# Kernel tuning notes

Measured on AMD Instinct MI355X. Metric: run time of the kernel, lower is better.

## Reference

```python
import jax, jax.numpy as jnp
import numpy as np

N, E = 50000, 800000
IN_C, HID, HEADS, NUM_CLASSES = 256, 64, 4, 10
LRELU_SLOPE = 0.2
LN_EPS = 1e-5


def setup_inputs() -> dict:
    key = jax.random.key(0)
    ks = jax.random.split(key, 12)
    HC = HEADS * HID
    glorot = lambda k, shp: jax.random.normal(k, shp, jnp.float32) * np.sqrt(2.0 / (shp[0] + shp[-1]))
    return {
        "x": jax.random.normal(ks[0], (N, IN_C), jnp.float32),
        "edge_index": jax.random.randint(ks[1], (2, E), 0, N, jnp.int64),
        "edge_weight": jax.random.uniform(ks[2], (E, 1), jnp.float32),
        "W": glorot(ks[3], (IN_C, HC)),
        "att_src": glorot(ks[4], (1, HEADS, HID)),
        "att_dst": glorot(ks[5], (1, HEADS, HID)),
        "att_edge": glorot(ks[6], (1, HEADS, HID)),
        "W_edge": glorot(ks[7], (1, HC)),
        "bias": jnp.zeros((HC,), jnp.float32),
        "ln_gamma": jnp.ones((HC,), jnp.float32),
        "ln_beta": jnp.zeros((HC,), jnp.float32),
        "fc_W": glorot(ks[8], (HC, NUM_CLASSES)),
        "fc_b": jnp.zeros((NUM_CLASSES,), jnp.float32),
    }


def reference(x, edge_index, edge_weight, W, att_src, att_dst, att_edge,
              W_edge, bias, ln_gamma, ln_beta, fc_W, fc_b):
    n = x.shape[0]
    src, dst = edge_index[0], edge_index[1]

    # GATConv: linear projection -> [N, H, C]
    xh = (x @ W).reshape(n, HEADS, HID)
    a_src = jnp.sum(xh * att_src, axis=-1)  # [N, H]
    a_dst = jnp.sum(xh * att_dst, axis=-1)  # [N, H]

    # edge feature projection (edge_dim=1) -> per-edge attention term
    eh = (edge_weight @ W_edge).reshape(-1, HEADS, HID)  # [E, H, C]
    a_edge = jnp.sum(eh * att_edge, axis=-1)             # [E, H]

    alpha = a_src[src] + a_dst[dst] + a_edge             # [E, H]
    alpha = jax.nn.leaky_relu(alpha, LRELU_SLOPE)

    # segment softmax over incoming edges of each destination node
    amax = jax.ops.segment_max(alpha, dst, num_segments=n)  # [N, H]
    amax = jnp.where(jnp.isfinite(amax), amax, 0.0)
    ex = jnp.exp(alpha - amax[dst])
    esum = jax.ops.segment_sum(ex, dst, num_segments=n)     # [N, H]
    attn = ex / (esum[dst] + 1e-16)                          # [E, H]

    # message = gathered source features weighted by attention; scatter-add
    msg = xh[src] * attn[:, :, None]                          # [E, H, C]
    out = jax.ops.segment_sum(msg, dst, num_segments=n)      # [N, H, C]
    out = out.reshape(n, HEADS * HID) + bias                  # concat heads

    # LayerNorm + ReLU (dropout is identity in eval) + Linear head
    mu = jnp.mean(out, axis=-1, keepdims=True)
    var = jnp.mean(jnp.square(out - mu), axis=-1, keepdims=True)
    out = (out - mu) * jax.lax.rsqrt(var + LN_EPS) * ln_gamma + ln_beta
    out = jax.nn.relu(out)
    return out @ fc_W + fc_b
```

## Files before the change

kernel.cpp:

```cpp
#include <hip/hip_runtime.h>
#include <hip/hip_bf16.h>

static constexpr int HEADS = 4;
static constexpr int HID   = 64;
static constexpr int HC    = 256;
static constexpr int NCLS  = 10;

typedef short bf16x8 __attribute__((ext_vector_type(8)));
typedef float f32x4  __attribute__((ext_vector_type(4)));
typedef _Float16 f16x4 __attribute__((ext_vector_type(4)));

__device__ inline unsigned short f2bf(float f) {
    union { float f; unsigned u; } c; c.f = f;
    unsigned r = (c.u + 0x7fff + ((c.u >> 16) & 1)) >> 16;
    return (unsigned short)r;
}
__device__ inline unsigned short f2h(float f) {
    _Float16 h = (_Float16)f; unsigned short u; __builtin_memcpy(&u, &h, 2); return u;
}
__device__ inline float h2f(unsigned short u) {
    _Float16 h; __builtin_memcpy(&h, &u, 2); return (float)h;
}

__global__ void prep_kernel(const float* __restrict__ We, const float* __restrict__ attE,
                            float* __restrict__ cE, const float* __restrict__ W,
                            unsigned short* __restrict__ Wt, const float* __restrict__ fcW,
                            float* __restrict__ fcWt) {
    int b = blockIdx.x, t = threadIdx.x;
    if (b == 0) {
        float p = We[t] * attE[t];
#pragma unroll
        for (int d = 32; d; d >>= 1) p += __shfl_xor(p, d, 64);
        if ((t & 63) == 0) cE[t >> 6] = p;
    } else if (b <= 256) {
        int k = b - 1;
        Wt[t * 256 + k] = f2bf(W[k * 256 + t]);
    } else {
        int j = b - 257;
        fcWt[j * HC + t] = fcW[t * NCLS + j];
    }
}

__global__ __launch_bounds__(256) void gemm_mfma(const float* __restrict__ X,
                                                 const unsigned short* __restrict__ Bt,
                                                 unsigned short* __restrict__ XHh, int M) {
    __shared__ alignas(16) unsigned short As[128][40];
    __shared__ alignas(16) unsigned short Bs[128][40];
    const int tid = threadIdx.x;
    const int lane = tid & 63, wid = tid >> 6;
    const int wr = wid >> 1, wc = wid & 1;
    const int bm = blockIdx.x * 128, bn = blockIdx.y * 128;
    const int fr = lane & 15, kg = lane >> 4;

    f32x4 acc[4][4] = {};

    for (int k0 = 0; k0 < 256; k0 += 32) {
        __syncthreads();
#pragma unroll
        for (int ss = 0; ss < 4; ++ss) {
            int idx = tid + (ss << 8);
            int row = idx >> 3, seg = idx & 7;
            int grow = bm + row;
            float4 av = make_float4(0.f, 0.f, 0.f, 0.f);
            if (grow < M) av = *(const float4*)&X[(size_t)grow * 256 + k0 + seg * 4];
            ushort4 ab = make_ushort4(f2bf(av.x), f2bf(av.y), f2bf(av.z), f2bf(av.w));
            *(ushort4*)&As[row][seg * 4] = ab;
        }
#pragma unroll
        for (int qq = 0; qq < 2; ++qq) {
            int q = tid + (qq << 8);
            int row = q >> 2, part = q & 3;
            const ushort4* bp = (const ushort4*)&Bt[(size_t)(bn + row) * 256 + k0 + part * 8];
            *(ushort4*)&Bs[row][part * 8]     = bp[0];
            *(ushort4*)&Bs[row][part * 8 + 4] = bp[1];
        }
        __syncthreads();

        bf16x8 af[4], bf[4];
#pragma unroll
        for (int i = 0; i < 4; ++i)
            af[i] = *(const bf16x8*)&As[wr * 64 + i * 16 + fr][kg * 8];
#pragma unroll
        for (int j = 0; j < 4; ++j)
            bf[j] = *(const bf16x8*)&Bs[wc * 64 + j * 16 + fr][kg * 8];
#pragma unroll
        for (int i = 0; i < 4; ++i)
#pragma unroll
            for (int j = 0; j < 4; ++j)
                acc[i][j] = __builtin_amdgcn_mfma_f32_16x16x32_bf16(af[i], bf[j], acc[i][j], 0, 0, 0);
    }

#pragma unroll
    for (int i = 0; i < 4; ++i) {
#pragma unroll
        for (int j = 0; j < 4; ++j) {
            int col = bn + wc * 64 + j * 16 + fr;
#pragma unroll
            for (int r = 0; r < 4; ++r) {
                int row = bm + wr * 64 + i * 16 + kg * 4 + r;
                if (row < M) XHh[(size_t)row * 256 + col] = f2h(acc[i][j][r]);
            }
        }
    }
}

__global__ __launch_bounds__(256) void attn_coef(const unsigned short* __restrict__ xhh,
                                                 const float* __restrict__ attS,
                                                 const float* __restrict__ attD,
                                                 float* __restrict__ a_src,
                                                 float* __restrict__ a_dst,
                                                 int Nn) {
    int wid = threadIdx.x >> 6, lane = threadIdx.x & 63;
    int n = blockIdx.x * 4 + wid;
    if (n >= Nn) return;
    ushort4 xv = *(const ushort4*)&xhh[(size_t)n * HC + lane * 4];
    float x0 = h2f(xv.x), x1 = h2f(xv.y), x2 = h2f(xv.z), x3 = h2f(xv.w);
    float4 sv = *(const float4*)&attS[lane * 4];
    float4 dv = *(const float4*)&attD[lane * 4];
    float ps = x0 * sv.x + x1 * sv.y + x2 * sv.z + x3 * sv.w;
    float pd = x0 * dv.x + x1 * dv.y + x2 * dv.z + x3 * dv.w;
#pragma unroll
    for (int d = 1; d < 16; d <<= 1) {
        ps += __shfl_xor(ps, d, 64);
        pd += __shfl_xor(pd, d, 64);
    }
    if ((lane & 15) == 0) {
        a_src[n * 4 + (lane >> 4)] = ps;
        a_dst[n * 4 + (lane >> 4)] = pd;
    }
}

__global__ void hist_kernel(const int* __restrict__ dst, int* __restrict__ deg, int E) {
    int e = blockIdx.x * 256 + threadIdx.x;
    if (e < E) atomicAdd(&deg[dst[e]], 1);
}

__global__ __launch_bounds__(1024) void scan1(const int* __restrict__ deg,
                                              int* __restrict__ row_start,
                                              int* __restrict__ bsum, int n) {
    __shared__ int wsum[16];
    const int tid = threadIdx.x, lane = tid & 63, wid = tid >> 6;
    int i = blockIdx.x * 1024 + tid;
    int v = (i < n) ? ((deg[i] + 3) & ~3) : 0;
    int incl = v;
#pragma unroll
    for (int d = 1; d < 64; d <<= 1) {
        int t = __shfl_up(incl, d, 64);
        if (lane >= d) incl += t;
    }
    if (lane == 63) wsum[wid] = incl;
    __syncthreads();
    if (tid < 16) {
        int w = wsum[tid];
#pragma unroll
        for (int d = 1; d < 16; d <<= 1) {
            int t = __shfl_up(w, d, 16);
            if (tid >= d) w += t;
        }
        wsum[tid] = w;
    }
    __syncthreads();
    int waveoff = wid ? wsum[wid - 1] : 0;
    if (i < n) row_start[i] = waveoff + incl - v;
    if (tid == 1023) bsum[blockIdx.x] = waveoff + incl;
}

__global__ __launch_bounds__(1024) void scan23(int* __restrict__ row_start,
                                               const int* __restrict__ bsum,
                                               int* __restrict__ cursor, int n, int nb) {
    __shared__ int pref[64];
    const int tid = threadIdx.x;
    if (tid < 64) {
        int v = (tid < nb) ? bsum[tid] : 0;
#pragma unroll
        for (int d = 1; d < 64; d <<= 1) {
            int t = __shfl_up(v, d, 64);
            if (tid >= d) v += t;
        }
        pref[tid] = v;
    }
    __syncthreads();
    int add = blockIdx.x ? pref[blockIdx.x - 1] : 0;
    int i = blockIdx.x * 1024 + tid;
    if (i < n) {
        int v = row_start[i] + add;
        row_start[i] = v;
        cursor[i] = v;
    }
    if (i == n) row_start[n] = pref[nb - 1];
}

__global__ void scatter_p(const int* __restrict__ src, const int* __restrict__ dst,
                          const float* __restrict__ ew, const float* __restrict__ a_src,
                          const float* __restrict__ a_dst, const float* __restrict__ cE,
                          int* __restrict__ cursor, int* __restrict__ srcs,
                          float* __restrict__ pq, int E) {
    int e = blockIdx.x * 256 + threadIdx.x;
    if (e >= E) return;
    int s = src[e], d = dst[e];
    float w = ew[e];
    float4 as_ = *(const float4*)&a_src[s * 4];
    float4 ad_ = *(const float4*)&a_dst[d * 4];
    float4 ce  = *(const float4*)cE;
    int pos = atomicAdd(&cursor[d], 1);
    srcs[pos] = s;
    float al[4] = {as_.x + ad_.x + ce.x * w, as_.y + ad_.y + ce.y * w,
                   as_.z + ad_.z + ce.z * w, as_.w + ad_.w + ce.w * w};
    float* base = pq + ((size_t)(pos >> 2)) * 16 + (pos & 3);
#pragma unroll
    for (int h = 0; h < 4; ++h) {
        float a = al[h] > 0.f ? al[h] : 0.2f * al[h];
        base[h * 4] = __expf(a);
    }
}

__global__ __launch_bounds__(256) void gat_main(
    const unsigned short* __restrict__ xhh, const int* __restrict__ row_start,
    const int* __restrict__ srcs, const float* __restrict__ pq,
    const float* __restrict__ bias, const float* __restrict__ gamma,
    const float* __restrict__ beta, const float* __restrict__ fcWt,
    const float* __restrict__ fcb, float* __restrict__ out, int Nn) {
    const int lane = threadIdx.x & 63, wid = threadIdx.x >> 6;
    const int n = blockIdx.x * 4 + wid;
    if (n >= Nn) return;
    const int myh = lane >> 4;
    const int rs = row_start[n], re = row_start[n + 1];

    f32x4 acc = {0.f, 0.f, 0.f, 0.f};
    float psum = 0.f;

    if (rs < re) {
        int4   sv = *(const int4*)&srcs[rs];
        float4 pv = *(const float4*)&pq[((size_t)(rs >> 2)) * 16 + myh * 4];
        for (int e0 = rs; e0 < re; e0 += 4) {
            int e1 = e0 + 4;
            int4 svn = sv; float4 pvn = pv;
            if (e1 < re) {
                svn = *(const int4*)&srcs[e1];
                pvn = *(const float4*)&pq[((size_t)(e1 >> 2)) * 16 + myh * 4];
            }
            psum += ((pv.x + pv.y) + (pv.z + pv.w));
            {
                int sb = __builtin_amdgcn_readfirstlane(sv.x);
                f16x4 xv = *(const f16x4*)(xhh + (size_t)sb * HC + lane * 4);
                acc[0] = fmaf(pv.x, (float)xv.x, acc[0]);
                acc[1] = fmaf(pv.x, (float)xv.y, acc[1]);
                acc[2] = fmaf(pv.x, (float)xv.z, acc[2]);
                acc[3] = fmaf(pv.x, (float)xv.w, acc[3]);
            }
            {
                int sb = __builtin_amdgcn_readfirstlane(sv.y);
                f16x4 xv = *(const f16x4*)(xhh + (size_t)sb * HC + lane * 4);
                acc[0] = fmaf(pv.y, (float)xv.x, acc[0]);
                acc[1] = fmaf(pv.y, (float)xv.y, acc[1]);
                acc[2] = fmaf(pv.y, (float)xv.z, acc[2]);
                acc[3] = fmaf(pv.y, (float)xv.w, acc[3]);
            }
            {
                int sb = __builtin_amdgcn_readfirstlane(sv.z);
                f16x4 xv = *(const f16x4*)(xhh + (size_t)sb * HC + lane * 4);
                acc[0] = fmaf(pv.z, (float)xv.x, acc[0]);
                acc[1] = fmaf(pv.z, (float)xv.y, acc[1]);
                acc[2] = fmaf(pv.z, (float)xv.z, acc[2]);
                acc[3] = fmaf(pv.z, (float)xv.w, acc[3]);
            }
            {
                int sb = __builtin_amdgcn_readfirstlane(sv.w);
                f16x4 xv = *(const f16x4*)(xhh + (size_t)sb * HC + lane * 4);
                acc[0] = fmaf(pv.w, (float)xv.x, acc[0]);
                acc[1] = fmaf(pv.w, (float)xv.y, acc[1]);
                acc[2] = fmaf(pv.w, (float)xv.z, acc[2]);
                acc[3] = fmaf(pv.w, (float)xv.w, acc[3]);
            }
            sv = svn; pv = pvn;
        }
    }

    float rin = 1.f / (psum + 1e-16f);

    float4 bv = *(const float4*)&bias[lane * 4];
    float v0 = acc[0] * rin + bv.x;
    float v1 = acc[1] * rin + bv.y;
    float v2 = acc[2] * rin + bv.z;
    float v3 = acc[3] * rin + bv.w;

    float s1 = v0 + v1 + v2 + v3;
    float s2 = v0 * v0 + v1 * v1 + v2 * v2 + v3 * v3;
#pragma unroll
    for (int d = 1; d < 64; d <<= 1) {
        s1 += __shfl_xor(s1, d, 64);
        s2 += __shfl_xor(s2, d, 64);
    }
    float mu = s1 * (1.f / 256.f);
    float var = s2 * (1.f / 256.f) - mu * mu;
    float rstd = rsqrtf(var + 1e-5f);
    float4 gv = *(const float4*)&gamma[lane * 4];
    float4 btv = *(const float4*)&beta[lane * 4];
    float y0 = fmaxf((v0 - mu) * rstd * gv.x + btv.x, 0.f);
    float y1 = fmaxf((v1 - mu) * rstd * gv.y + btv.y, 0.f);
    float y2 = fmaxf((v2 - mu) * rstd * gv.z + btv.z, 0.f);
    float y3 = fmaxf((v3 - mu) * rstd * gv.w + btv.w, 0.f);

    float keep = 0.f;
#pragma unroll
    for (int j = 0; j < NCLS; ++j) {
        float4 wv = *(const float4*)&fcWt[j * HC + lane * 4];
        float pj = y0 * wv.x;
        pj = fmaf(y1, wv.y, pj);
        pj = fmaf(y2, wv.z, pj);
        pj = fmaf(y3, wv.w, pj);
#pragma unroll
        for (int d = 1; d < 64; d <<= 1) pj += __shfl_xor(pj, d, 64);
        if (lane == j) keep = pj + fcb[j];
    }
    if (lane < NCLS) out[n * NCLS + lane] = keep;
}

extern "C" void kernel_launch(void* const* d_in, const int* in_sizes, int n_in,
                              void* d_out, int out_size, void* d_ws, size_t ws_size,
                              hipStream_t stream) {
    const float* x    = (const float*)d_in[0];
    const int*   ei   = (const int*)d_in[1];
    const float* ew   = (const float*)d_in[2];
    const float* W    = (const float*)d_in[3];
    const float* attS = (const float*)d_in[4];
    const float* attD = (const float*)d_in[5];
    const float* attE = (const float*)d_in[6];
    const float* We   = (const float*)d_in[7];
    const float* bias = (const float*)d_in[8];
    const float* gam  = (const float*)d_in[9];
    const float* bet  = (const float*)d_in[10];
    const float* fcW  = (const float*)d_in[11];
    const float* fcb  = (const float*)d_in[12];
    float* out = (float*)d_out;

    const int Nn = in_sizes[0] / HC;
    const int E  = in_sizes[1] / 2;
    const int* src = ei;
    const int* dst = ei + E;
    const int nb = (Nn + 1023) / 1024;
    const int EpMax = E + 4 * Nn;

    char* ws = (char*)d_ws;
    size_t off = 0;
    auto alloc = [&](size_t bytes) { void* p = ws + off; off = (off + bytes + 255) & ~size_t(255); return p; };
    unsigned short* xhh  = (unsigned short*)alloc((size_t)Nn * HC * 2);
    unsigned short* wt   = (unsigned short*)alloc((size_t)HC * HC * 2);
    float* a_srcb    = (float*)alloc((size_t)Nn * 4 * 4);
    float* a_dstb    = (float*)alloc((size_t)Nn * 4 * 4);
    float* cE        = (float*)alloc(256);
    float* fcWt      = (float*)alloc((size_t)NCLS * HC * 4);
    int*   row_start = (int*)  alloc((size_t)(Nn + 1) * 4);
    int*   deg       = (int*)  alloc((size_t)Nn * 4);
    int*   cursor    = (int*)  alloc((size_t)Nn * 4);
    int*   bsum      = (int*)  alloc((size_t)nb * 4);
    int*   srcs     = (int*)  alloc((size_t)EpMax * 4);
    float* pq       = (float*)alloc((size_t)EpMax * 16);
    (void)ws_size;

    hipMemsetAsync(deg, 0, (size_t)Nn * 4, stream);
    size_t zspan = (size_t)((char*)pq - (char*)srcs) + (size_t)EpMax * 16;
    hipMemsetAsync(srcs, 0, zspan, stream);

    prep_kernel<<<267, 256, 0, stream>>>(We, attE, cE, W, wt, fcW, fcWt);

    dim3 g((Nn + 127) / 128, 2);
    gemm_mfma<<<g, 256, 0, stream>>>(x, wt, xhh, Nn);

    attn_coef<<<(Nn + 3) / 4, 256, 0, stream>>>(xhh, attS, attD, a_srcb, a_dstb, Nn);
    hist_kernel<<<(E + 255) / 256, 256, 0, stream>>>(dst, deg, E);
    scan1<<<nb, 1024, 0, stream>>>(deg, row_start, bsum, Nn);
    scan23<<<nb, 1024, 0, stream>>>(row_start, bsum, cursor, Nn, nb);
    scatter_p<<<(E + 255) / 256, 256, 0, stream>>>(src, dst, ew, a_srcb, a_dstb, cE,
                                                   cursor, srcs, pq, E);
    gat_main<<<(Nn + 3) / 4, 256, 0, stream>>>(xhh, row_start, srcs, pq,
                                               bias, gam, bet, fcWt, fcb, out, Nn);
}
```

Measured before the change: 220.1 us.

## Precompute edge ranks, pipeline gathers, drop memset, split FC into MFMA kernel

The histogram pass now records each edge's rank within its destination, so the scatter computes slot positions without a second atomic pass, and the cursor array goes away. The large memset of srcs/pq is removed, and the tail of each padded row is handled by masking instead. The gather loop is restructured into a two-stage software pipeline that prefetches the next 4-edge chunk's features and the metadata two chunks ahead. The per-node FC reduction, which used ten wave-wide shuffle reductions, is replaced by writing fp16 LayerNorm output and running a separate MFMA GEMM kernel. This costs an extra 25MB round trip for yh and fp16 rounding of the activations.

```diff
diff --git a/kernel.cpp b/kernel.cpp
--- a/kernel.cpp
+++ b/kernel.cpp
@@ -6,9 +6,10 @@
 static constexpr int HC    = 256;
 static constexpr int NCLS  = 10;
 
-typedef short bf16x8 __attribute__((ext_vector_type(8)));
-typedef float f32x4  __attribute__((ext_vector_type(4)));
-typedef _Float16 f16x4 __attribute__((ext_vector_type(4)));
+typedef short    bf16x8 __attribute__((ext_vector_type(8)));
+typedef _Float16 f16x8  __attribute__((ext_vector_type(8)));
+typedef _Float16 f16x4  __attribute__((ext_vector_type(4)));
+typedef float    f32x4  __attribute__((ext_vector_type(4)));
 
 __device__ inline unsigned short f2bf(float f) {
     union { float f; unsigned u; } c; c.f = f;
@@ -25,7 +26,7 @@
 __global__ void prep_kernel(const float* __restrict__ We, const float* __restrict__ attE,
                             float* __restrict__ cE, const float* __restrict__ W,
                             unsigned short* __restrict__ Wt, const float* __restrict__ fcW,
-                            float* __restrict__ fcWt) {
+                            unsigned short* __restrict__ fcWh) {
     int b = blockIdx.x, t = threadIdx.x;
     if (b == 0) {
         float p = We[t] * attE[t];
@@ -37,7 +38,9 @@
         Wt[t * 256 + k] = f2bf(W[k * 256 + t]);
     } else {
         int j = b - 257;
-        fcWt[j * HC + t] = fcW[t * NCLS + j];
+        unsigned short v = 0;
+        if (j < NCLS) v = f2h(fcW[t * NCLS + j]);
+        fcWh[j * 256 + t] = v;
     }
 }
 
@@ -130,9 +133,10 @@
     }
 }
 
-__global__ void hist_kernel(const int* __restrict__ dst, int* __restrict__ deg, int E) {
+__global__ void hist_kernel(const int* __restrict__ dst, int* __restrict__ deg,
+                            int* __restrict__ rank, int E) {
     int e = blockIdx.x * 256 + threadIdx.x;
-    if (e < E) atomicAdd(&deg[dst[e]], 1);
+    if (e < E) rank[e] = atomicAdd(&deg[dst[e]], 1);
 }
 
 __global__ __launch_bounds__(1024) void scan1(const int* __restrict__ deg,
@@ -166,8 +170,7 @@
 }
 
 __global__ __launch_bounds__(1024) void scan23(int* __restrict__ row_start,
-                                               const int* __restrict__ bsum,
-                                               int* __restrict__ cursor, int n, int nb) {
+                                               const int* __restrict__ bsum, int n, int nb) {
     __shared__ int pref[64];
     const int tid = threadIdx.x;
     if (tid < 64) {
@@ -182,19 +185,15 @@
     __syncthreads();
     int add = blockIdx.x ? pref[blockIdx.x - 1] : 0;
     int i = blockIdx.x * 1024 + tid;
-    if (i < n) {
-        int v = row_start[i] + add;
-        row_start[i] = v;
-        cursor[i] = v;
-    }
+    if (i < n) row_start[i] += add;
     if (i == n) row_start[n] = pref[nb - 1];
 }
 
 __global__ void scatter_p(const int* __restrict__ src, const int* __restrict__ dst,
                           const float* __restrict__ ew, const float* __restrict__ a_src,
                           const float* __restrict__ a_dst, const float* __restrict__ cE,
-                          int* __restrict__ cursor, int* __restrict__ srcs,
-                          float* __restrict__ pq, int E) {
+                          const int* __restrict__ row_start, const int* __restrict__ rank,
+                          int* __restrict__ srcs, float* __restrict__ pq, int E) {
     int e = blockIdx.x * 256 + threadIdx.x;
     if (e >= E) return;
     int s = src[e], d = dst[e];
@@ -202,7 +201,7 @@
     float4 as_ = *(const float4*)&a_src[s * 4];
     float4 ad_ = *(const float4*)&a_dst[d * 4];
     float4 ce  = *(const float4*)cE;
-    int pos = atomicAdd(&cursor[d], 1);
+    int pos = row_start[d] + rank[e];
     srcs[pos] = s;
     float al[4] = {as_.x + ad_.x + ce.x * w, as_.y + ad_.y + ce.y * w,
                    as_.z + ad_.z + ce.z * w, as_.w + ad_.w + ce.w * w};
@@ -216,65 +215,82 @@
 
 __global__ __launch_bounds__(256) void gat_main(
     const unsigned short* __restrict__ xhh, const int* __restrict__ row_start,
-    const int* __restrict__ srcs, const float* __restrict__ pq,
-    const float* __restrict__ bias, const float* __restrict__ gamma,
-    const float* __restrict__ beta, const float* __restrict__ fcWt,
-    const float* __restrict__ fcb, float* __restrict__ out, int Nn) {
+    const int* __restrict__ deg, const int* __restrict__ srcs,
+    const float* __restrict__ pq, const float* __restrict__ bias,
+    const float* __restrict__ gamma, const float* __restrict__ beta,
+    unsigned short* __restrict__ yh, int Nn) {
     const int lane = threadIdx.x & 63, wid = threadIdx.x >> 6;
     const int n = blockIdx.x * 4 + wid;
     if (n >= Nn) return;
     const int myh = lane >> 4;
-    const int rs = row_start[n], re = row_start[n + 1];
+    const int rs = row_start[n];
+    const int dn = deg[n];
+    const int nfull = dn >> 2, rem = dn & 3;
+    const unsigned short* xl = xhh + (size_t)lane * 4;
 
     f32x4 acc = {0.f, 0.f, 0.f, 0.f};
     float psum = 0.f;
 
-    if (rs < re) {
-        int4   sv = *(const int4*)&srcs[rs];
-        float4 pv = *(const float4*)&pq[((size_t)(rs >> 2)) * 16 + myh * 4];
-        for (int e0 = rs; e0 < re; e0 += 4) {
-            int e1 = e0 + 4;
-            int4 svn = sv; float4 pvn = pv;
-            if (e1 < re) {
-                svn = *(const int4*)&srcs[e1];
-                pvn = *(const float4*)&pq[((size_t)(e1 >> 2)) * 16 + myh * 4];
-            }
-            psum += ((pv.x + pv.y) + (pv.z + pv.w));
-            {
-                int sb = __builtin_amdgcn_readfirstlane(sv.x);
-                f16x4 xv = *(const f16x4*)(xhh + (size_t)sb * HC + lane * 4);
-                acc[0] = fmaf(pv.x, (float)xv.x, acc[0]);
-                acc[1] = fmaf(pv.x, (float)xv.y, acc[1]);
-                acc[2] = fmaf(pv.x, (float)xv.z, acc[2]);
-                acc[3] = fmaf(pv.x, (float)xv.w, acc[3]);
-            }
-            {
-                int sb = __builtin_amdgcn_readfirstlane(sv.y);
-                f16x4 xv = *(const f16x4*)(xhh + (size_t)sb * HC + lane * 4);
-                acc[0] = fmaf(pv.y, (float)xv.x, acc[0]);
-                acc[1] = fmaf(pv.y, (float)xv.y, acc[1]);
-                acc[2] = fmaf(pv.y, (float)xv.z, acc[2]);
-                acc[3] = fmaf(pv.y, (float)xv.w, acc[3]);
-            }
-            {
-                int sb = __builtin_amdgcn_readfirstlane(sv.z);
-                f16x4 xv = *(const f16x4*)(xhh + (size_t)sb * HC + lane * 4);
-                acc[0] = fmaf(pv.z, (float)xv.x, acc[0]);
-                acc[1] = fmaf(pv.z, (float)xv.y, acc[1]);
-                acc[2] = fmaf(pv.z, (float)xv.z, acc[2]);
-                acc[3] = fmaf(pv.z, (float)xv.w, acc[3]);
-            }
-            {
-                int sb = __builtin_amdgcn_readfirstlane(sv.w);
-                f16x4 xv = *(const f16x4*)(xhh + (size_t)sb * HC + lane * 4);
-                acc[0] = fmaf(pv.w, (float)xv.x, acc[0]);
-                acc[1] = fmaf(pv.w, (float)xv.y, acc[1]);
-                acc[2] = fmaf(pv.w, (float)xv.z, acc[2]);
-                acc[3] = fmaf(pv.w, (float)xv.w, acc[3]);
-            }
-            sv = svn; pv = pvn;
-        }
-    }
+#define LOADMETA(c, S, P)                                                     \
+    S = *(const int4*)&srcs[rs + (c) * 4];                                    \
+    P = *(const float4*)&pq[((size_t)((rs >> 2) + (c))) * 16 + myh * 4];
+#define GATHER(S, X0, X1, X2, X3)                                             \
+    X0 = *(const f16x4*)(xl + (size_t)__builtin_amdgcn_readfirstlane((S).x) * HC); \
+    X1 = *(const f16x4*)(xl + (size_t)__builtin_amdgcn_readfirstlane((S).y) * HC); \
+    X2 = *(const f16x4*)(xl + (size_t)__builtin_amdgcn_readfirstlane((S).z) * HC); \
+    X3 = *(const f16x4*)(xl + (size_t)__builtin_amdgcn_readfirstlane((S).w) * HC);
+#define COMPUTE(P, X0, X1, X2, X3)                                            \
+    psum += ((P).x + (P).y) + ((P).z + (P).w);                                \
+    acc[0] = fmaf((P).x, (float)(X0).x, acc[0]);                              \
+    acc[1] = fmaf((P).x, (float)(X0).y, acc[1]);                              \
+    acc[2] = fmaf((P).x, (float)(X0).z, acc[2]);                              \
+    acc[3] = fmaf((P).x, (float)(X0).w, acc[3]);                              \
+    acc[0] = fmaf((P).y, (float)(X1).x, acc[0]);                              \
+    acc[1] = fmaf((P).y, (float)(X1).y, acc[1]);                              \
+    acc[2] = fmaf((P).y, (float)(X1).z, acc[2]);                              \
+    acc[3] = fmaf((P).y, (float)(X1).w, acc[3]);                              \
+    acc[0] = fmaf((P).z, (float)(X2).x, acc[0]);                              \
+    acc[1] = fmaf((P).z, (float)(X2).y, acc[1]);                              \
+    acc[2] = fmaf((P).z, (float)(X2).z, acc[2]);                              \
+    acc[3] = fmaf((P).z, (float)(X2).w, acc[3]);                              \
+    acc[0] = fmaf((P).w, (float)(X3).x, acc[0]);                              \
+    acc[1] = fmaf((P).w, (float)(X3).y, acc[1]);                              \
+    acc[2] = fmaf((P).w, (float)(X3).z, acc[2]);                              \
+    acc[3] = fmaf((P).w, (float)(X3).w, acc[3]);
+
+    if (nfull > 0) {
+        int4 s0, sN = {0, 0, 0, 0}, s2 = {0, 0, 0, 0};
+        float4 pC, pN = {0.f, 0.f, 0.f, 0.f}, p2 = {0.f, 0.f, 0.f, 0.f};
+        f16x4 g0, g1, g2, g3;
+        LOADMETA(0, s0, pC);
+        GATHER(s0, g0, g1, g2, g3);
+        if (nfull > 1) { LOADMETA(1, sN, pN); }
+        for (int c = 0; c < nfull; ++c) {
+            f16x4 h0, h1, h2, h3;
+            if (c + 1 < nfull) { GATHER(sN, h0, h1, h2, h3); }
+            if (c + 2 < nfull) { LOADMETA(c + 2, s2, p2); }
+            COMPUTE(pC, g0, g1, g2, g3);
+            pC = pN; pN = p2; sN = s2;
+            g0 = h0; g1 = h1; g2 = h2; g3 = h3;
+        }
+    }
+    if (rem) {
+        int4 s; float4 p;
+        LOADMETA(nfull, s, p);
+        p.w = 0.f;
+        if (rem < 3) p.z = 0.f;
+        if (rem < 2) p.y = 0.f;
+        int b0 = __builtin_amdgcn_readfirstlane(s.x);
+        int b1 = rem > 1 ? __builtin_amdgcn_readfirstlane(s.y) : b0;
+        int b2 = rem > 2 ? __builtin_amdgcn_readfirstlane(s.z) : b0;
+        f16x4 x0 = *(const f16x4*)(xl + (size_t)b0 * HC);
+        f16x4 x1 = *(const f16x4*)(xl + (size_t)b1 * HC);
+        f16x4 x2 = *(const f16x4*)(xl + (size_t)b2 * HC);
+        COMPUTE(p, x0, x1, x2, x0);
+    }
+#undef LOADMETA
+#undef GATHER
+#undef COMPUTE
 
     float rin = 1.f / (psum + 1e-16f);
 
@@ -285,14 +301,14 @@
     float v3 = acc[3] * rin + bv.w;
 
     float s1 = v0 + v1 + v2 + v3;
-    float s2 = v0 * v0 + v1 * v1 + v2 * v2 + v3 * v3;
+    float s2v = v0 * v0 + v1 * v1 + v2 * v2 + v3 * v3;
 #pragma unroll
     for (int d = 1; d < 64; d <<= 1) {
         s1 += __shfl_xor(s1, d, 64);
-        s2 += __shfl_xor(s2, d, 64);
+        s2v += __shfl_xor(s2v, d, 64);
     }
     float mu = s1 * (1.f / 256.f);
-    float var = s2 * (1.f / 256.f) - mu * mu;
+    float var = s2v * (1.f / 256.f) - mu * mu;
     float rstd = rsqrtf(var + 1e-5f);
     float4 gv = *(const float4*)&gamma[lane * 4];
     float4 btv = *(const float4*)&beta[lane * 4];
@@ -301,19 +317,41 @@
     float y2 = fmaxf((v2 - mu) * rstd * gv.z + btv.z, 0.f);
     float y3 = fmaxf((v3 - mu) * rstd * gv.w + btv.w, 0.f);
 
-    float keep = 0.f;
-#pragma unroll
-    for (int j = 0; j < NCLS; ++j) {
-        float4 wv = *(const float4*)&fcWt[j * HC + lane * 4];
-        float pj = y0 * wv.x;
-        pj = fmaf(y1, wv.y, pj);
-        pj = fmaf(y2, wv.z, pj);
-        pj = fmaf(y3, wv.w, pj);
-#pragma unroll
-        for (int d = 1; d < 64; d <<= 1) pj += __shfl_xor(pj, d, 64);
-        if (lane == j) keep = pj + fcb[j];
-    }
-    if (lane < NCLS) out[n * NCLS + lane] = keep;
+    f16x4 yv;
+    yv.x = (_Float16)y0; yv.y = (_Float16)y1; yv.z = (_Float16)y2; yv.w = (_Float16)y3;
+    *(f16x4*)&yh[(size_t)n * HC + lane * 4] = yv;
+}
+
+__global__ __launch_bounds__(256) void fc_gemm(const unsigned short* __restrict__ yh,
+                                               const unsigned short* __restrict__ fcWh,
+                                               const float* __restrict__ fcb,
+                                               float* __restrict__ out, int M) {
+    const int lane = threadIdx.x & 63, wid = threadIdx.x >> 6;
+    const int rowbase = blockIdx.x * 256 + wid * 64;
+    const int fr = lane & 15, kg = lane >> 4;
+    f32x4 acc[4] = {};
+#pragma unroll
+    for (int k0 = 0; k0 < 256; k0 += 32) {
+        f16x8 bfr = *(const f16x8*)&fcWh[fr * 256 + k0 + kg * 8];
+#pragma unroll
+        for (int i = 0; i < 4; ++i) {
+            int row = rowbase + i * 16 + fr;
+            f16x8 afr = {};
+            if (row < M) afr = *(const f16x8*)&yh[(size_t)row * 256 + k0 + kg * 8];
+            acc[i] = __builtin_amdgcn_mfma_f32_16x16x32_f16(afr, bfr, acc[i], 0, 0, 0);
+        }
+    }
+    if (fr < NCLS) {
+        float bb = fcb[fr];
+#pragma unroll
+        for (int i = 0; i < 4; ++i) {
+#pragma unroll
+            for (int r = 0; r < 4; ++r) {
+                int row = rowbase + i * 16 + kg * 4 + r;
+                if (row < M) out[(size_t)row * NCLS + fr] = acc[i][r] + bb;
+            }
+        }
+    }
 }
 
 extern "C" void kernel_launch(void* const* d_in, const int* in_sizes, int n_in,
@@ -345,34 +383,34 @@
     size_t off = 0;
     auto alloc = [&](size_t bytes) { void* p = ws + off; off = (off + bytes + 255) & ~size_t(255); return p; };
     unsigned short* xhh  = (unsigned short*)alloc((size_t)Nn * HC * 2);
+    unsigned short* yh   = (unsigned short*)alloc((size_t)Nn * HC * 2);
     unsigned short* wt   = (unsigned short*)alloc((size_t)HC * HC * 2);
+    unsigned short* fcWh = (unsigned short*)alloc((size_t)16 * HC * 2);
     float* a_srcb    = (float*)alloc((size_t)Nn * 4 * 4);
     float* a_dstb    = (float*)alloc((size_t)Nn * 4 * 4);
     float* cE        = (float*)alloc(256);
-    float* fcWt      = (float*)alloc((size_t)NCLS * HC * 4);
     int*   row_start = (int*)  alloc((size_t)(Nn + 1) * 4);
     int*   deg       = (int*)  alloc((size_t)Nn * 4);
-    int*   cursor    = (int*)  alloc((size_t)Nn * 4);
     int*   bsum      = (int*)  alloc((size_t)nb * 4);
-    int*   srcs     = (int*)  alloc((size_t)EpMax * 4);
-    float* pq       = (float*)alloc((size_t)EpMax * 16);
+    int*   rank      = (int*)  alloc((size_t)E * 4);
+    int*   srcs      = (int*)  alloc((size_t)EpMax * 4);
+    float* pq        = (float*)alloc((size_t)EpMax * 16);
     (void)ws_size;
 
     hipMemsetAsync(deg, 0, (size_t)Nn * 4, stream);
-    size_t zspan = (size_t)((char*)pq - (char*)srcs) + (size_t)EpMax * 16;
-    hipMemsetAsync(srcs, 0, zspan, stream);
-
-    prep_kernel<<<267, 256, 0, stream>>>(We, attE, cE, W, wt, fcW, fcWt);
+
+    prep_kernel<<<273, 256, 0, stream>>>(We, attE, cE, W, wt, fcW, fcWh);
 
     dim3 g((Nn + 127) / 128, 2);
     gemm_mfma<<<g, 256, 0, stream>>>(x, wt, xhh, Nn);
 
     attn_coef<<<(Nn + 3) / 4, 256, 0, stream>>>(xhh, attS, attD, a_srcb, a_dstb, Nn);
-    hist_kernel<<<(E + 255) / 256, 256, 0, stream>>>(dst, deg, E);
+    hist_kernel<<<(E + 255) / 256, 256, 0, stream>>>(dst, deg, rank, E);
     scan1<<<nb, 1024, 0, stream>>>(deg, row_start, bsum, Nn);
-    scan23<<<nb, 1024, 0, stream>>>(row_start, bsum, cursor, Nn, nb);
+    scan23<<<nb, 1024, 0, stream>>>(row_start, bsum, Nn, nb);
     scatter_p<<<(E + 255) / 256, 256, 0, stream>>>(src, dst, ew, a_srcb, a_dstb, cE,
-                                                   cursor, srcs, pq, E);
-    gat_main<<<(Nn + 3) / 4, 256, 0, stream>>>(xhh, row_start, srcs, pq,
-                                               bias, gam, bet, fcWt, fcb, out, Nn);
-}
+                                                   row_start, rank, srcs, pq, E);
+    gat_main<<<(Nn + 3) / 4, 256, 0, stream>>>(xhh, row_start, deg, srcs, pq,
+                                               bias, gam, bet, yh, Nn);
+    fc_gemm<<<(Nn + 255) / 256, 256, 0, stream>>>(yh, fcWh, fcb, out, Nn);
+}
```

After: 202.1 us. 8.2% less time.
